# Optimization experiments

Measured on AMD Instinct MI355X. Metric: run time of the kernel, lower is better.

## Reference

```python
import jax, jax.numpy as jnp
import numpy as np

D_MODEL = 256; D_FF = 512; D_STATE = 16; D_CONV = 4; EXPAND = 2
D_INNER = EXPAND * D_MODEL          # 512
DT_RANK = (D_MODEL + 15) // 16      # 16
BSZ = 16; NVARS = 32; PATCH_NUM = 64


def setup_inputs() -> dict:
    key = jax.random.key(0)
    ks = jax.random.split(key, 16)
    def nrm(k, shape, scale=0.02):
        return jax.random.normal(k, shape, jnp.float32) * scale
    inp = {}
    inp["x"] = jax.random.normal(ks[0], (BSZ, NVARS, D_MODEL, PATCH_NUM), jnp.float32)
    # Mamba block params
    inp["in_proj_w"] = nrm(ks[1], (2 * D_INNER, D_MODEL))
    inp["in_proj_b"] = jnp.zeros((2 * D_INNER,), jnp.float32)
    inp["conv_w"] = nrm(ks[2], (D_INNER, D_CONV), 0.1)   # depthwise causal conv
    inp["conv_b"] = jnp.zeros((D_INNER,), jnp.float32)
    inp["x_proj_w"] = nrm(ks[3], (DT_RANK + 2 * D_STATE, D_INNER))
    inp["dt_proj_w"] = nrm(ks[4], (D_INNER, DT_RANK))
    inp["dt_proj_b"] = nrm(ks[5], (D_INNER,), 0.1)
    inp["A_log"] = jnp.log(jnp.broadcast_to(
        jnp.arange(1, D_STATE + 1, dtype=jnp.float32), (D_INNER, D_STATE)))
    inp["Dp"] = jnp.ones((D_INNER,), jnp.float32)
    inp["out_proj_w"] = nrm(ks[6], (D_MODEL, D_INNER))
    # Mamba_ffn norms + pointwise FFN
    inp["norm1_g"] = jnp.ones((D_MODEL,), jnp.float32)
    inp["norm1_b"] = jnp.zeros((D_MODEL,), jnp.float32)
    inp["ffn1_w"] = nrm(ks[7], (D_FF, D_MODEL))
    inp["ffn1_b"] = jnp.zeros((D_FF,), jnp.float32)
    inp["ffn2_w"] = nrm(ks[8], (D_MODEL, D_FF))
    inp["ffn2_b"] = jnp.zeros((D_MODEL,), jnp.float32)
    inp["norm2_g"] = jnp.ones((D_MODEL,), jnp.float32)
    inp["norm2_b"] = jnp.zeros((D_MODEL,), jnp.float32)
    # outer VarPatch LayerNorm
    inp["ln_g"] = jnp.ones((D_MODEL,), jnp.float32)
    inp["ln_b"] = jnp.zeros((D_MODEL,), jnp.float32)
    return inp


def layer_norm(x, g, b, eps=1e-5):
    mu = x.mean(-1, keepdims=True)
    var = ((x - mu) ** 2).mean(-1, keepdims=True)
    return (x - mu) * jax.lax.rsqrt(var + eps) * g + b


def mamba(x, in_proj_w, in_proj_b, conv_w, conv_b, x_proj_w,
          dt_proj_w, dt_proj_b, A_log, Dp, out_proj_w):
    # x: (b, L, d_model)
    b, L, _ = x.shape
    xz = x @ in_proj_w.T + in_proj_b            # (b, L, 2*d_inner)
    xi, z = jnp.split(xz, 2, axis=-1)           # each (b, L, d_inner)
    # causal depthwise conv along L
    xc = xi.transpose(0, 2, 1)                  # (b, d_inner, L)
    xc = jax.lax.conv_general_dilated(
        xc, conv_w[:, None, :], (1,), [(D_CONV - 1, 0)],
        dimension_numbers=("NCH", "OIH", "NCH"),
        feature_group_count=D_INNER) + conv_b[None, :, None]
    xi = jax.nn.silu(xc.transpose(0, 2, 1))     # (b, L, d_inner)
    x_dbl = xi @ x_proj_w.T                     # (b, L, dt_rank + 2*n)
    dt = x_dbl[..., :DT_RANK]
    B = x_dbl[..., DT_RANK:DT_RANK + D_STATE]
    C = x_dbl[..., DT_RANK + D_STATE:]
    delta = jax.nn.softplus(dt @ dt_proj_w.T + dt_proj_b)   # (b, L, d_inner)
    A = -jnp.exp(A_log)                         # (d_inner, n)

    def step(h, inp):
        d_t, B_t, C_t, u_t = inp                # (b,d),(b,n),(b,n),(b,d)
        dA = jnp.exp(d_t[..., None] * A)        # (b, d, n)
        h = dA * h + (d_t * u_t)[..., None] * B_t[:, None, :]
        y = jnp.einsum("bdn,bn->bd", h, C_t)
        return h, y

    h0 = jnp.zeros((b, D_INNER, D_STATE), xi.dtype)
    xs = (delta.transpose(1, 0, 2), B.transpose(1, 0, 2),
          C.transpose(1, 0, 2), xi.transpose(1, 0, 2))
    _, ys = jax.lax.scan(step, h0, xs)          # ys: (L, b, d_inner)
    y = ys.transpose(1, 0, 2) + xi * Dp
    y = y * jax.nn.silu(z)
    return y @ out_proj_w.T                     # (b, L, d_model)


def reference(x, in_proj_w, in_proj_b, conv_w, conv_b, x_proj_w,
              dt_proj_w, dt_proj_b, A_log, Dp, out_proj_w,
              norm1_g, norm1_b, ffn1_w, ffn1_b, ffn2_w, ffn2_b,
              norm2_g, norm2_b, ln_g, ln_b):
    b, nv, dm, pn = x.shape
    x_residual = x
    h = x.reshape(b, pn * nv, dm)               # same flat view as torch reshape
    # Mamba_ffn: mamba + residual, norm, pointwise FFN + residual, norm
    h = h + mamba(h, in_proj_w, in_proj_b, conv_w, conv_b, x_proj_w,
                  dt_proj_w, dt_proj_b, A_log, Dp, out_proj_w)
    h = layer_norm(h, norm1_g, norm1_b)
    y = jax.nn.relu(h @ ffn1_w.T + ffn1_b)      # 1x1 conv == linear
    y = y @ ffn2_w.T + ffn2_b
    h = layer_norm(h + y, norm2_g, norm2_b)
    # back to patches
    h = h.reshape(b, nv, pn, dm)
    h = layer_norm(h, ln_g, ln_b).transpose(0, 1, 3, 2)   # (b, nv, dm, pn)
    return h + x_residual
```

## Files before the change

kernel.cpp:

```cpp
#include <hip/hip_runtime.h>
#include <hip/hip_bf16.h>
#include <math.h>

#define SEQ    2048
#define NBTOT  16
#define NCH    64
#define CHL    32

#define L2E 1.4426950408889634f

typedef __attribute__((ext_vector_type(8))) __bf16 bf16x8;
typedef __attribute__((ext_vector_type(4))) float f32x4;
typedef __attribute__((ext_vector_type(2))) float f32x2;

#define GLOAD16(gp, lp)                                                   \
  __builtin_amdgcn_global_load_lds(                                       \
      (const __attribute__((address_space(1))) unsigned int*)(gp),        \
      (__attribute__((address_space(3))) unsigned int*)(lp), 16, 0, 0)

__device__ __forceinline__ float exp2_(float x) {
  return __builtin_amdgcn_exp2f(x);
}
__device__ __forceinline__ float silu_(float x) {
  return x * __builtin_amdgcn_rcpf(1.f + exp2_(-x * L2E));
}
__device__ __forceinline__ float softplus_(float x) {
  return fmaxf(x, 0.f) + __logf(1.f + exp2_(-fabsf(x) * L2E));
}
__device__ __forceinline__ float wsum_(float v) {
#pragma unroll
  for (int off = 32; off > 0; off >>= 1) v += __shfl_xor(v, off, 64);
  return v;
}
__device__ __forceinline__ int xcdswz_(int bid, int nwg) {
  return (bid & 7) * (nwg >> 3) + (bid >> 3);
}
__device__ __forceinline__ void powpairs_(float e1, f32x2 p[8]) {
  float e2 = e1 * e1;
  f32x2 p0; p0.x = e1; p0.y = e2;
  f32x2 s2; s2.x = e2; s2.y = e2;
  f32x2 s4 = s2 * s2;
  f32x2 s8 = s4 * s4;
  p[0] = p0;      p[1] = p0 * s2; p[2] = p0 * s4; p[3] = p[1] * s4;
  p[4] = p0 * s8; p[5] = p[1] * s8; p[6] = p[2] * s8; p[7] = p[3] * s8;
}

template <bool BIAS, bool RELU, bool RES, bool RESB, bool F32OUT, bool BF16OUT,
          int NTLOG>
__global__ __launch_bounds__(256) void gemm_bf16(
    const __hip_bfloat16* __restrict__ A, const __hip_bfloat16* __restrict__ W,
    const float* __restrict__ bias, const float* __restrict__ res,
    const __hip_bfloat16* __restrict__ resb, float* __restrict__ C,
    __hip_bfloat16* __restrict__ Cb, int N, int K) {
  __shared__ __align__(16) char ShRaw[36864];
  short* Als = reinterpret_cast<short*>(ShRaw);
  short* Bls = Als + 8192;
  const int tid = threadIdx.x;
  const int lane = tid & 63;
  const int wid = tid >> 6;
  const int swz = xcdswz_(blockIdx.x, gridDim.x);
  const int m0 = (swz >> NTLOG) * 128;
  const int n0 = (swz & ((1 << NTLOG) - 1)) * 128;
  const int wm = (wid >> 1) * 64;
  const int wn = (wid & 1) * 64;
  const int lr = lane & 15;
  const int lk = lane >> 4;

  f32x4 acc[4][4];
#pragma unroll
  for (int m = 0; m < 4; ++m)
#pragma unroll
    for (int n = 0; n < 4; ++n) acc[m][n] = (f32x4){0.f, 0.f, 0.f, 0.f};

  const int srow = wid * 32 + (lane >> 3);
  const int scol = (lane & 7) * 8;
  const __hip_bfloat16* Ag = A + (size_t)(m0 + srow) * K + scol;
  const __hip_bfloat16* Wg = W + (size_t)(n0 + srow) * K + scol;
  short* Alb = Als + wid * 2048;
  short* Blb = Bls + wid * 2048;

  for (int kt = 0; kt < K; kt += 64) {
#pragma unroll
    for (int i = 0; i < 4; ++i) {
      GLOAD16(Ag + (size_t)(i * 8) * K + kt, Alb + i * 512);
      GLOAD16(Wg + (size_t)(i * 8) * K + kt, Blb + i * 512);
    }
    __syncthreads();
    const bf16x8* Af = reinterpret_cast<const bf16x8*>(Als);
    const bf16x8* Bf = reinterpret_cast<const bf16x8*>(Bls);
#pragma unroll
    for (int ks = 0; ks < 2; ++ks) {
      bf16x8 av[4], bv[4];
#pragma unroll
      for (int m = 0; m < 4; ++m)
        av[m] = Af[(wm + m * 16 + lr) * 8 + ks * 4 + lk];
#pragma unroll
      for (int n = 0; n < 4; ++n)
        bv[n] = Bf[(wn + n * 16 + lr) * 8 + ks * 4 + lk];
#pragma unroll
      for (int m = 0; m < 4; ++m)
#pragma unroll
        for (int n = 0; n < 4; ++n)
          acc[m][n] = __builtin_amdgcn_mfma_f32_16x16x32_bf16(
              av[m], bv[n], acc[m][n], 0, 0, 0);
    }
    __syncthreads();
  }

  if (BF16OUT) {
    __hip_bfloat16* epi =
        reinterpret_cast<__hip_bfloat16*>(ShRaw) + wid * 4608;
#pragma unroll
    for (int n = 0; n < 4; ++n) {
      int col = n0 + wn + n * 16 + lr;
      float bval = BIAS ? bias[col] : 0.f;
#pragma unroll
      for (int m = 0; m < 4; ++m) {
        int lrow = m * 16 + lk * 4;
#pragma unroll
        for (int r = 0; r < 4; ++r) {
          float v = acc[m][n][r];
          if (BIAS) v += bval;
          if (RES) v += res[(size_t)(m0 + wm + lrow + r) * N + col];
          if (RESB)
            v += __bfloat162float(resb[(size_t)(m0 + wm + lrow + r) * N + col]);
          if (RELU) v = fmaxf(v, 0.f);
          epi[(lrow + r) * 72 + n * 16 + lr] = __float2bfloat16(v);
        }
      }
    }
    const int lr8 = (lane & 7) * 8;
    const int lrw = lane >> 3;
    const size_t obase = (size_t)(m0 + wm) * N + n0 + wn + lr8;
#pragma unroll
    for (int j = 0; j < 8; ++j) {
      int row = j * 8 + lrw;
      int4 vv = *reinterpret_cast<const int4*>(epi + row * 72 + lr8);
      *reinterpret_cast<int4*>(&Cb[obase + (size_t)row * N]) = vv;
    }
  }
  if (F32OUT) {
#pragma unroll
    for (int n = 0; n < 4; ++n) {
      int col = n0 + wn + n * 16 + lr;
      if (col >= N) continue;
      float bval = BIAS ? bias[col] : 0.f;
#pragma unroll
      for (int m = 0; m < 4; ++m) {
        int row0 = m0 + wm + m * 16 + lk * 4;
#pragma unroll
        for (int r = 0; r < 4; ++r) {
          size_t off = (size_t)(row0 + r) * N + col;
          float v = acc[m][n][r];
          if (BIAS) v += bval;
          if (RES) v += res[off];
          if (RESB) v += __bfloat162float(resb[off]);
          if (RELU) v = fmaxf(v, 0.f);
          C[off] = v;
        }
      }
    }
  }
}

__global__ __launch_bounds__(256) void cast_bf16_k(
    const float* __restrict__ src, __hip_bfloat16* __restrict__ dst, int n4) {
  int i = xcdswz_(blockIdx.x, gridDim.x) * 256 + threadIdx.x;
  if (i >= n4) return;
  float4 v = reinterpret_cast<const float4*>(src)[i];
  union { __hip_bfloat16 h[4]; short4 s4; } u;
  u.h[0] = __float2bfloat16(v.x); u.h[1] = __float2bfloat16(v.y);
  u.h[2] = __float2bfloat16(v.z); u.h[3] = __float2bfloat16(v.w);
  reinterpret_cast<short4*>(dst)[i] = u.s4;
}

__global__ __launch_bounds__(256) void pad_wx_k(
    const float* __restrict__ src, __hip_bfloat16* __restrict__ dst) {
  int i = blockIdx.x * 256 + threadIdx.x;
  int row = i >> 7;
  union { __hip_bfloat16 h[4]; short4 s4; } u;
  if (row < 48) {
    float4 v = reinterpret_cast<const float4*>(src)[i];
    u.h[0] = __float2bfloat16(v.x); u.h[1] = __float2bfloat16(v.y);
    u.h[2] = __float2bfloat16(v.z); u.h[3] = __float2bfloat16(v.w);
  } else {
    u.h[0] = u.h[1] = u.h[2] = u.h[3] = __float2bfloat16(0.f);
  }
  reinterpret_cast<short4*>(dst)[i] = u.s4;
}

__global__ __launch_bounds__(256) void conv_silu_k(
    const __hip_bfloat16* __restrict__ xz, const float* __restrict__ cw,
    const float* __restrict__ cb, __hip_bfloat16* __restrict__ xi) {
  int idx = xcdswz_(blockIdx.x, gridDim.x) * 256 + threadIdx.x;
  int t = idx & 63;
  int r = idx >> 6;
  int l = r & (SEQ - 1);
  int c8 = t << 3;
  const __hip_bfloat16* p = xz + (size_t)r * 1024 + c8;
  union U8 { int4 v; __hip_bfloat16 h[8]; } x0, x1, x2, x3, o;
  const int4 z4 = make_int4(0, 0, 0, 0);
  x3.v = *reinterpret_cast<const int4*>(p);
  x2.v = (l >= 1) ? *reinterpret_cast<const int4*>(p - 1024) : z4;
  x1.v = (l >= 2) ? *reinterpret_cast<const int4*>(p - 2048) : z4;
  x0.v = (l >= 3) ? *reinterpret_cast<const int4*>(p - 3072) : z4;
  const float4* cw4 = reinterpret_cast<const float4*>(cw);
#pragma unroll
  for (int j = 0; j < 8; ++j) {
    float4 w = cw4[c8 + j];
    float acc = cb[c8 + j];
    acc = fmaf(w.x, __bfloat162float(x0.h[j]), acc);
    acc = fmaf(w.y, __bfloat162float(x1.h[j]), acc);
    acc = fmaf(w.z, __bfloat162float(x2.h[j]), acc);
    acc = fmaf(w.w, __bfloat162float(x3.h[j]), acc);
    o.h[j] = __float2bfloat16(silu_(acc));
  }
  reinterpret_cast<int4*>(xi)[idx] = o.v;
}

__global__ __launch_bounds__(256) void scan_p1(
    const __hip_bfloat16* __restrict__ u, const float* __restrict__ xdbl,
    const float* __restrict__ A_log, const float* __restrict__ wdt,
    const float* __restrict__ bdt, float* __restrict__ dlsum,
    __hip_bfloat16* __restrict__ hp, __hip_bfloat16* __restrict__ deltab) {
  const int w = xcdswz_(blockIdx.x, gridDim.x);
  const int b = w >> 7;
  const int c = (w >> 1) & 63;
  const int d = ((w & 1) << 8) + threadIdx.x;
  const int l0 = c * CHL;
  float A2[16];
  f32x2 w2[8];
  {
    const float4* aq = reinterpret_cast<const float4*>(&A_log[d * 16]);
    const f32x2* wq = reinterpret_cast<const f32x2*>(&wdt[d * 16]);
#pragma unroll
    for (int q = 0; q < 4; ++q) {
      float4 v = aq[q];
      A2[q * 4 + 0] = -exp2_(v.x * L2E) * L2E;
      A2[q * 4 + 1] = -exp2_(v.y * L2E) * L2E;
      A2[q * 4 + 2] = -exp2_(v.z * L2E) * L2E;
      A2[q * 4 + 3] = -exp2_(v.w * L2E) * L2E;
    }
#pragma unroll
    for (int k = 0; k < 8; ++k) w2[k] = wq[k];
  }
  bool chainok = true;
#pragma unroll
  for (int n = 1; n < 16; ++n)
    chainok = chainok &&
              (fabsf(A2[n] - (float)(n + 1) * A2[0]) <=
               1e-4f * (float)(n + 1) * fabsf(A2[0]));
  const float bdtd = bdt[d];
  const float nL = A2[0];
  f32x2 h2[8];
#pragma unroll
  for (int k = 0; k < 8; ++k) h2[k] = (f32x2){0.f, 0.f};
  float dls = 0.f;
  size_t base = (size_t)(b * SEQ + l0) * 512 + d;
  const float* rowp = xdbl + (size_t)(b * SEQ + l0) * 48;
  if (chainok) {
#pragma unroll 4
    for (int i = 0; i < CHL; ++i) {
      const f32x2* r2 = reinterpret_cast<const f32x2*>(rowp + i * 48);
      f32x2 acc2; acc2.x = bdtd; acc2.y = 0.f;
#pragma unroll
      for (int k = 0; k < 8; ++k)
        acc2 = __builtin_elementwise_fma(r2[k], w2[k], acc2);
      float dl = softplus_(acc2.x + acc2.y);
      deltab[base + (size_t)i * 512] = __float2bfloat16(dl);
      dls += dl;
      float du = dl * __bfloat162float(u[base + (size_t)i * 512]);
      f32x2 p[8];
      powpairs_(exp2_(dl * nL), p);
      f32x2 du2; du2.x = du; du2.y = du;
#pragma unroll
      for (int k = 0; k < 8; ++k)
        h2[k] = __builtin_elementwise_fma(p[k], h2[k], du2 * r2[8 + k]);
    }
  } else {
#pragma unroll 2
    for (int i = 0; i < CHL; ++i) {
      const f32x2* r2 = reinterpret_cast<const f32x2*>(rowp + i * 48);
      f32x2 acc2; acc2.x = bdtd; acc2.y = 0.f;
#pragma unroll
      for (int k = 0; k < 8; ++k)
        acc2 = __builtin_elementwise_fma(r2[k], w2[k], acc2);
      float dl = softplus_(acc2.x + acc2.y);
      deltab[base + (size_t)i * 512] = __float2bfloat16(dl);
      dls += dl;
      float du = dl * __bfloat162float(u[base + (size_t)i * 512]);
      f32x2 du2; du2.x = du; du2.y = du;
#pragma unroll
      for (int k = 0; k < 8; ++k) {
        f32x2 a; a.x = exp2_(dl * A2[2 * k]); a.y = exp2_(dl * A2[2 * k + 1]);
        h2[k] = __builtin_elementwise_fma(a, h2[k], du2 * r2[8 + k]);
      }
    }
  }
  size_t sc = (size_t)(b * NCH + c) * 512 + d;
  dlsum[sc] = dls;
  union { __hip_bfloat16 h[4]; short4 s4; } o0, o1, o2, o3;
#pragma unroll
  for (int j = 0; j < 2; ++j) {
    o0.h[2*j] = __float2bfloat16(h2[j].x);   o0.h[2*j+1] = __float2bfloat16(h2[j].y);
    o1.h[2*j] = __float2bfloat16(h2[2+j].x); o1.h[2*j+1] = __float2bfloat16(h2[2+j].y);
    o2.h[2*j] = __float2bfloat16(h2[4+j].x); o2.h[2*j+1] = __float2bfloat16(h2[4+j].y);
    o3.h[2*j] = __float2bfloat16(h2[6+j].x); o3.h[2*j+1] = __float2bfloat16(h2[6+j].y);
  }
  short4* hq = reinterpret_cast<short4*>(hp + sc * 16);
  hq[0] = o0.s4; hq[1] = o1.s4; hq[2] = o2.s4; hq[3] = o3.s4;
}

__global__ __launch_bounds__(256) void scan_p2(
    __hip_bfloat16* hp, const float* __restrict__ dlsum,
    const float* __restrict__ A_log) {
  int g = xcdswz_(blockIdx.x, gridDim.x) * 256 + threadIdx.x;
  int b = g >> 13;
  int dn = g & 8191;
  int d = dn >> 4;
  float A2n = -exp2_(A_log[dn] * L2E) * L2E;
  float H = 0.f;
  for (int c = 0; c < NCH; ++c) {
    float ds = dlsum[(size_t)(b * NCH + c) * 512 + d];
    size_t idx = (size_t)(b * NCH + c) * 8192 + dn;
    float p = __bfloat162float(hp[idx]);
    float a = exp2_(A2n * ds);
    hp[idx] = __float2bfloat16(H);
    H = fmaf(a, H, p);
  }
}

__global__ __launch_bounds__(256) void scan_p3(
    const __hip_bfloat16* u,
    const float* __restrict__ A_log,
    const __hip_bfloat16* __restrict__ deltab, const float* __restrict__ xdbl,
    const __hip_bfloat16* __restrict__ Hc, const float* __restrict__ Dp,
    const __hip_bfloat16* __restrict__ xz, __hip_bfloat16* y) {
  const int w = xcdswz_(blockIdx.x, gridDim.x);
  const int b = w >> 7;
  const int c = (w >> 1) & 63;
  const int d = ((w & 1) << 8) + threadIdx.x;
  const int l0 = c * CHL;
  float A2[16];
  {
    const float4* aq = reinterpret_cast<const float4*>(&A_log[d * 16]);
#pragma unroll
    for (int q = 0; q < 4; ++q) {
      float4 v = aq[q];
      A2[q * 4 + 0] = -exp2_(v.x * L2E) * L2E;
      A2[q * 4 + 1] = -exp2_(v.y * L2E) * L2E;
      A2[q * 4 + 2] = -exp2_(v.z * L2E) * L2E;
      A2[q * 4 + 3] = -exp2_(v.w * L2E) * L2E;
    }
  }
  bool chainok = true;
#pragma unroll
  for (int n = 1; n < 16; ++n)
    chainok = chainok &&
              (fabsf(A2[n] - (float)(n + 1) * A2[0]) <=
               1e-4f * (float)(n + 1) * fabsf(A2[0]));
  const float nL = A2[0];
  f32x2 h2[8];
  {
    const short4* hq =
        reinterpret_cast<const short4*>(Hc + ((size_t)(b * NCH + c) * 512 + d) * 16);
#pragma unroll
    for (int q = 0; q < 4; ++q) {
      union { short4 s4; __hip_bfloat16 h[4]; } iv;
      iv.s4 = hq[q];
      h2[2*q].x = __bfloat162float(iv.h[0]);
      h2[2*q].y = __bfloat162float(iv.h[1]);
      h2[2*q+1].x = __bfloat162float(iv.h[2]);
      h2[2*q+1].y = __bfloat162float(iv.h[3]);
    }
  }
  const float Dpd = Dp[d];
  size_t base = (size_t)(b * SEQ + l0) * 512 + d;
  const float* rowp = xdbl + (size_t)(b * SEQ + l0) * 48;
  const __hip_bfloat16* zp = xz + (size_t)(b * SEQ + l0) * 1024 + 512 + d;
  if (chainok) {
#pragma unroll 4
    for (int i = 0; i < CHL; ++i) {
      const f32x2* r2 = reinterpret_cast<const f32x2*>(rowp + i * 48);
      float dl = __bfloat162float(deltab[base + (size_t)i * 512]);
      float ul = __bfloat162float(u[base + (size_t)i * 512]);
      float du = dl * ul;
      f32x2 p[8];
      powpairs_(exp2_(dl * nL), p);
      f32x2 du2; du2.x = du; du2.y = du;
      f32x2 yv2; yv2.x = 0.f; yv2.y = 0.f;
#pragma unroll
      for (int k = 0; k < 8; ++k) {
        h2[k] = __builtin_elementwise_fma(p[k], h2[k], du2 * r2[8 + k]);
        yv2 = __builtin_elementwise_fma(h2[k], r2[16 + k], yv2);
      }
      float yv = yv2.x + yv2.y;
      float zv = __bfloat162float(zp[(size_t)i * 1024]);
      y[base + (size_t)i * 512] =
          __float2bfloat16((yv + ul * Dpd) * silu_(zv));
    }
  } else {
#pragma unroll 2
    for (int i = 0; i < CHL; ++i) {
      const f32x2* r2 = reinterpret_cast<const f32x2*>(rowp + i * 48);
      float dl = __bfloat162float(deltab[base + (size_t)i * 512]);
      float ul = __bfloat162float(u[base + (size_t)i * 512]);
      float du = dl * ul;
      f32x2 du2; du2.x = du; du2.y = du;
      f32x2 yv2; yv2.x = 0.f; yv2.y = 0.f;
#pragma unroll
      for (int k = 0; k < 8; ++k) {
        f32x2 a; a.x = exp2_(dl * A2[2 * k]); a.y = exp2_(dl * A2[2 * k + 1]);
        h2[k] = __builtin_elementwise_fma(a, h2[k], du2 * r2[8 + k]);
        yv2 = __builtin_elementwise_fma(h2[k], r2[16 + k], yv2);
      }
      float yv = yv2.x + yv2.y;
      float zv = __bfloat162float(zp[(size_t)i * 1024]);
      y[base + (size_t)i * 512] =
          __float2bfloat16((yv + ul * Dpd) * silu_(zv));
    }
  }
}

__global__ __launch_bounds__(256) void ln_k(
    const __hip_bfloat16* __restrict__ in, const float* __restrict__ g,
    const float* __restrict__ bb, __hip_bfloat16* __restrict__ outb) {
  int row = (xcdswz_(blockIdx.x, gridDim.x) * 256 + threadIdx.x) >> 6;
  int lane = threadIdx.x & 63;
  union { short4 s4; __hip_bfloat16 h[4]; } iv;
  iv.s4 = reinterpret_cast<const short4*>(in)[row * 64 + lane];
  float v0 = __bfloat162float(iv.h[0]), v1 = __bfloat162float(iv.h[1]);
  float v2 = __bfloat162float(iv.h[2]), v3 = __bfloat162float(iv.h[3]);
  float mu = wsum_(v0 + v1 + v2 + v3) * (1.f / 256.f);
  float a0 = v0 - mu, a1 = v1 - mu, a2 = v2 - mu, a3 = v3 - mu;
  float var = wsum_(a0 * a0 + a1 * a1 + a2 * a2 + a3 * a3) * (1.f / 256.f);
  float rs = __builtin_amdgcn_rsqf(var + 1e-5f);
  float4 gg = *reinterpret_cast<const float4*>(&g[lane * 4]);
  float4 bq = *reinterpret_cast<const float4*>(&bb[lane * 4]);
  union { __hip_bfloat16 h[4]; short4 s4; } u;
  u.h[0] = __float2bfloat16(a0 * rs * gg.x + bq.x);
  u.h[1] = __float2bfloat16(a1 * rs * gg.y + bq.y);
  u.h[2] = __float2bfloat16(a2 * rs * gg.z + bq.z);
  u.h[3] = __float2bfloat16(a3 * rs * gg.w + bq.w);
  reinterpret_cast<short4*>(outb)[row * 64 + lane] = u.s4;
}

__global__ __launch_bounds__(256) void final_k(
    const __hip_bfloat16* __restrict__ t2, const float* __restrict__ g2v,
    const float* __restrict__ b2v, const float* __restrict__ g3v,
    const float* __restrict__ b3v, const float* __restrict__ x,
    float* __restrict__ out) {
  int bx = xcdswz_(blockIdx.x, gridDim.x);
  int half = bx & 1, nv = (bx >> 1) & 31, b = bx >> 6;
  int wave = threadIdx.x >> 6, lane = threadIdx.x & 63;
  __shared__ float sh[32][257];
  float4 gg2 = *reinterpret_cast<const float4*>(&g2v[lane * 4]);
  float4 bb2 = *reinterpret_cast<const float4*>(&b2v[lane * 4]);
  float4 gg3 = *reinterpret_cast<const float4*>(&g3v[lane * 4]);
  float4 bb3 = *reinterpret_cast<const float4*>(&b3v[lane * 4]);
#pragma unroll
  for (int i = 0; i < 8; ++i) {
    int pn = wave * 8 + i;
    int r = ((b * 32 + nv) << 6) + (half << 5) + pn;
    union { short4 s4; __hip_bfloat16 h[4]; } iv;
    iv.s4 = reinterpret_cast<const short4*>(t2)[r * 64 + lane];
    float v0 = __bfloat162float(iv.h[0]), v1 = __bfloat162float(iv.h[1]);
    float v2 = __bfloat162float(iv.h[2]), v3 = __bfloat162float(iv.h[3]);
    float mu = wsum_(v0 + v1 + v2 + v3) * (1.f / 256.f);
    float a0 = v0 - mu, a1 = v1 - mu, a2 = v2 - mu, a3 = v3 - mu;
    float var = wsum_(a0 * a0 + a1 * a1 + a2 * a2 + a3 * a3) * (1.f / 256.f);
    float rs = __builtin_amdgcn_rsqf(var + 1e-5f);
    a0 = a0 * rs * gg2.x + bb2.x; a1 = a1 * rs * gg2.y + bb2.y;
    a2 = a2 * rs * gg2.z + bb2.z; a3 = a3 * rs * gg2.w + bb2.w;
    mu = wsum_(a0 + a1 + a2 + a3) * (1.f / 256.f);
    float c0 = a0 - mu, c1 = a1 - mu, c2 = a2 - mu, c3 = a3 - mu;
    var = wsum_(c0 * c0 + c1 * c1 + c2 * c2 + c3 * c3) * (1.f / 256.f);
    rs = __builtin_amdgcn_rsqf(var + 1e-5f);
    sh[pn][lane * 4 + 0] = c0 * rs * gg3.x + bb3.x;
    sh[pn][lane * 4 + 1] = c1 * rs * gg3.y + bb3.y;
    sh[pn][lane * 4 + 2] = c2 * rs * gg3.z + bb3.z;
    sh[pn][lane * 4 + 3] = c3 * rs * gg3.w + bb3.w;
  }
  __syncthreads();
  int pnl = threadIdx.x & 31;
  int dbase = threadIdx.x >> 5;
  size_t obase = (size_t)((b * 32 + nv) * 256) * 64 + (half << 5) + pnl;
#pragma unroll
  for (int k = 0; k < 32; ++k) {
    int dd = dbase + (k << 3);
    size_t oi = obase + (size_t)dd * 64;
    out[oi] = sh[pnl][dd] + x[oi];
  }
}

extern "C" void kernel_launch(void* const* d_in, const int* in_sizes, int n_in,
                              void* d_out, int out_size, void* d_ws,
                              size_t ws_size, hipStream_t stream) {
  const float* x    = (const float*)d_in[0];
  const float* w_in = (const float*)d_in[1];
  const float* b_in = (const float*)d_in[2];
  const float* cw   = (const float*)d_in[3];
  const float* cb   = (const float*)d_in[4];
  const float* wx   = (const float*)d_in[5];
  const float* wdt  = (const float*)d_in[6];
  const float* bdt  = (const float*)d_in[7];
  const float* alog = (const float*)d_in[8];
  const float* Dp   = (const float*)d_in[9];
  const float* wout = (const float*)d_in[10];
  const float* g1   = (const float*)d_in[11];
  const float* b1   = (const float*)d_in[12];
  const float* wf1  = (const float*)d_in[13];
  const float* bf1  = (const float*)d_in[14];
  const float* wf2  = (const float*)d_in[15];
  const float* bf2  = (const float*)d_in[16];
  const float* g2   = (const float*)d_in[17];
  const float* b2   = (const float*)d_in[18];
  const float* g3   = (const float*)d_in[19];
  const float* b3   = (const float*)d_in[20];
  float* out = (float*)d_out;

  const size_t MB1 = 1048576;
  char* g = (char*)d_ws;
  __hip_bfloat16* wbf_in  = (__hip_bfloat16*)(g);
  __hip_bfloat16* wbf_out = (__hip_bfloat16*)(g + 524288);
  __hip_bfloat16* wbf_f1  = (__hip_bfloat16*)(g + 786432);
  __hip_bfloat16* wbf_f2  = (__hip_bfloat16*)(g + 1048576);
  __hip_bfloat16* wbf_xp  = (__hip_bfloat16*)(g + 1310720);
  const size_t SHARED = 1572864;

  const size_t PB = 11 * MB1 + 393216;
  int nb = (int)((ws_size - SHARED) / PB);
  if (ws_size <= SHARED || nb < 1) return;
  if (nb > NBTOT) nb = NBTOT;

  dim3 blk(256);
  cast_bf16_k<<<dim3(256), blk, 0, stream>>>(w_in, wbf_in, 65536);
  cast_bf16_k<<<dim3(128), blk, 0, stream>>>(wout, wbf_out, 32768);
  cast_bf16_k<<<dim3(128), blk, 0, stream>>>(wf1, wbf_f1, 32768);
  cast_bf16_k<<<dim3(128), blk, 0, stream>>>(wf2, wbf_f2, 32768);
  pad_wx_k<<<dim3(64), blk, 0, stream>>>(wx, wbf_xp);

  for (int b0 = 0; b0 < NBTOT; b0 += nb) {
    int bn = (NBTOT - b0 < nb) ? (NBTOT - b0) : nb;
    char* base = g + SHARED;
    char* RA = base;
    char* RB = base + (size_t)bn * 4 * MB1;
    char* RC = base + (size_t)bn * 5 * MB1;
    char* RD = base + (size_t)bn * 7 * MB1;
    char* RE = RD + (size_t)bn * 393216;
    char* RF = RE + (size_t)bn * 2 * MB1;

    __hip_bfloat16* xz     = (__hip_bfloat16*)RA;
    __hip_bfloat16* t2b    = (__hip_bfloat16*)RA;
    __hip_bfloat16* xbf    = (__hip_bfloat16*)RB;
    float*          dlsum  = (float*)RB;
    __hip_bfloat16* xibf   = (__hip_bfloat16*)RC;
    __hip_bfloat16* ffnybf = (__hip_bfloat16*)RC;
    float*          xdbl   = (float*)RD;
    __hip_bfloat16* hp     = (__hip_bfloat16*)RE;
    __hip_bfloat16* resb   = (__hip_bfloat16*)RE;
    __hip_bfloat16* h1bf   = (__hip_bfloat16*)(RE + (size_t)bn * MB1);
    __hip_bfloat16* deltab = (__hip_bfloat16*)RF;

    const float* xg = x + (size_t)b0 * SEQ * 256;
    float* outg = out + (size_t)b0 * SEQ * 256;
    int M = bn * SEQ;
    int MT = M / 128;

    cast_bf16_k<<<dim3(M * 64 / 256), blk, 0, stream>>>(xg, xbf, M * 64);
    gemm_bf16<true, false, false, false, false, true, 3>
        <<<dim3(8 * MT), blk, 0, stream>>>(xbf, wbf_in, b_in, nullptr, nullptr,
                                           nullptr, xz, 1024, 256);
    conv_silu_k<<<dim3(M / 4), blk, 0, stream>>>(xz, cw, cb, xibf);
    gemm_bf16<false, false, false, false, true, false, 0>
        <<<dim3(MT), blk, 0, stream>>>(xibf, wbf_xp, nullptr, nullptr,
                                       nullptr, xdbl, nullptr, 48, 512);
    scan_p1<<<dim3(bn * 128), blk, 0, stream>>>(xibf, xdbl, alog, wdt, bdt,
                                                dlsum, hp, deltab);
    scan_p2<<<dim3(bn * 32), blk, 0, stream>>>(hp, dlsum, alog);
    scan_p3<<<dim3(bn * 128), blk, 0, stream>>>(xibf, alog, deltab, xdbl,
                                                hp, Dp, xz, xibf);
    gemm_bf16<false, false, true, false, false, true, 1>
        <<<dim3(2 * MT), blk, 0, stream>>>(xibf, wbf_out, nullptr, xg, nullptr,
                                           nullptr, resb, 256, 512);
    ln_k<<<dim3(M / 4), blk, 0, stream>>>(resb, g1, b1, h1bf);
    gemm_bf16<true, true, false, false, false, true, 2>
        <<<dim3(4 * MT), blk, 0, stream>>>(h1bf, wbf_f1, bf1, nullptr, nullptr,
                                           nullptr, ffnybf, 512, 256);
    gemm_bf16<true, false, false, true, false, true, 1>
        <<<dim3(2 * MT), blk, 0, stream>>>(ffnybf, wbf_f2, bf2, nullptr, h1bf,
                                           nullptr, t2b, 256, 512);
    final_k<<<dim3(bn * 64), blk, 0, stream>>>(t2b, g2, b2, g3, b3, xg, outg);
  }
}
```

Measured before the change: 277.6 us.

## Fuse causal conv+SiLU into x_proj GEMM and scan kernels, drop xi buffer

Removes the standalone conv_silu kernel and its materialized bf16 xi tensor. The depthwise causal conv and SiLU are recomputed on the fly from xz inside a dedicated x_proj GEMM, which builds its A tile in registers, and inside both scan passes using a rolling three-tap window. This saves one kernel launch and a write plus reread of the xi activation. In exchange the conv is computed three times, and the x_proj GEMM loses async LDS loads for A.

```diff
diff --git a/kernel.cpp b/kernel.cpp
--- a/kernel.cpp
+++ b/kernel.cpp
@@ -45,12 +45,11 @@
   p[4] = p0 * s8; p[5] = p[1] * s8; p[6] = p[2] * s8; p[7] = p[3] * s8;
 }
 
-template <bool BIAS, bool RELU, bool RES, bool RESB, bool F32OUT, bool BF16OUT,
-          int NTLOG>
+template <bool BIAS, bool RELU, bool RES, bool RESB, bool BF16OUT, int NTLOG>
 __global__ __launch_bounds__(256) void gemm_bf16(
     const __hip_bfloat16* __restrict__ A, const __hip_bfloat16* __restrict__ W,
     const float* __restrict__ bias, const float* __restrict__ res,
-    const __hip_bfloat16* __restrict__ resb, float* __restrict__ C,
+    const __hip_bfloat16* __restrict__ resb,
     __hip_bfloat16* __restrict__ Cb, int N, int K) {
   __shared__ __align__(16) char ShRaw[36864];
   short* Als = reinterpret_cast<short*>(ShRaw);
@@ -107,58 +106,125 @@
     __syncthreads();
   }
 
-  if (BF16OUT) {
-    __hip_bfloat16* epi =
-        reinterpret_cast<__hip_bfloat16*>(ShRaw) + wid * 4608;
-#pragma unroll
-    for (int n = 0; n < 4; ++n) {
-      int col = n0 + wn + n * 16 + lr;
-      float bval = BIAS ? bias[col] : 0.f;
-#pragma unroll
-      for (int m = 0; m < 4; ++m) {
-        int lrow = m * 16 + lk * 4;
-#pragma unroll
-        for (int r = 0; r < 4; ++r) {
-          float v = acc[m][n][r];
-          if (BIAS) v += bval;
-          if (RES) v += res[(size_t)(m0 + wm + lrow + r) * N + col];
-          if (RESB)
-            v += __bfloat162float(resb[(size_t)(m0 + wm + lrow + r) * N + col]);
-          if (RELU) v = fmaxf(v, 0.f);
-          epi[(lrow + r) * 72 + n * 16 + lr] = __float2bfloat16(v);
-        }
+  __hip_bfloat16* epi = reinterpret_cast<__hip_bfloat16*>(ShRaw) + wid * 4608;
+#pragma unroll
+  for (int n = 0; n < 4; ++n) {
+    int col = n0 + wn + n * 16 + lr;
+    float bval = BIAS ? bias[col] : 0.f;
+#pragma unroll
+    for (int m = 0; m < 4; ++m) {
+      int lrow = m * 16 + lk * 4;
+#pragma unroll
+      for (int r = 0; r < 4; ++r) {
+        float v = acc[m][n][r];
+        if (BIAS) v += bval;
+        if (RES) v += res[(size_t)(m0 + wm + lrow + r) * N + col];
+        if (RESB)
+          v += __bfloat162float(resb[(size_t)(m0 + wm + lrow + r) * N + col]);
+        if (RELU) v = fmaxf(v, 0.f);
+        epi[(lrow + r) * 72 + n * 16 + lr] = __float2bfloat16(v);
       }
     }
-    const int lr8 = (lane & 7) * 8;
-    const int lrw = lane >> 3;
-    const size_t obase = (size_t)(m0 + wm) * N + n0 + wn + lr8;
-#pragma unroll
-    for (int j = 0; j < 8; ++j) {
-      int row = j * 8 + lrw;
-      int4 vv = *reinterpret_cast<const int4*>(epi + row * 72 + lr8);
-      *reinterpret_cast<int4*>(&Cb[obase + (size_t)row * N]) = vv;
-    }
-  }
-  if (F32OUT) {
-#pragma unroll
-    for (int n = 0; n < 4; ++n) {
-      int col = n0 + wn + n * 16 + lr;
-      if (col >= N) continue;
-      float bval = BIAS ? bias[col] : 0.f;
-#pragma unroll
-      for (int m = 0; m < 4; ++m) {
-        int row0 = m0 + wm + m * 16 + lk * 4;
-#pragma unroll
-        for (int r = 0; r < 4; ++r) {
-          size_t off = (size_t)(row0 + r) * N + col;
-          float v = acc[m][n][r];
-          if (BIAS) v += bval;
-          if (RES) v += res[off];
-          if (RESB) v += __bfloat162float(resb[off]);
-          if (RELU) v = fmaxf(v, 0.f);
-          C[off] = v;
-        }
+  }
+  const int lr8 = (lane & 7) * 8;
+  const int lrw = lane >> 3;
+  const size_t obase = (size_t)(m0 + wm) * N + n0 + wn + lr8;
+#pragma unroll
+  for (int j = 0; j < 8; ++j) {
+    int row = j * 8 + lrw;
+    int4 vv = *reinterpret_cast<const int4*>(epi + row * 72 + lr8);
+    *reinterpret_cast<int4*>(&Cb[obase + (size_t)row * N]) = vv;
+  }
+}
+
+__global__ __launch_bounds__(256) void gemm_xproj(
+    const __hip_bfloat16* __restrict__ xz, const __hip_bfloat16* __restrict__ W,
+    const float* __restrict__ cw, const float* __restrict__ cb,
+    float* __restrict__ C) {
+  __shared__ __align__(16) short Als[128 * 64];
+  __shared__ __align__(16) short Bls[128 * 64];
+  const int tid = threadIdx.x;
+  const int lane = tid & 63;
+  const int wid = tid >> 6;
+  const int m0 = xcdswz_(blockIdx.x, gridDim.x) * 128;
+  const int wm = (wid >> 1) * 64;
+  const int wn = (wid & 1) * 64;
+  const int lr = lane & 15;
+  const int lk = lane >> 4;
+
+  f32x4 acc[4][4];
+#pragma unroll
+  for (int m = 0; m < 4; ++m)
+#pragma unroll
+    for (int n = 0; n < 4; ++n) acc[m][n] = (f32x4){0.f, 0.f, 0.f, 0.f};
+
+  const int srow = wid * 32 + (lane >> 3);
+  const int scol = (lane & 7) * 8;
+  const __hip_bfloat16* Wg = W + (size_t)srow * 512 + scol;
+  short* Alb = Als + wid * 2048;
+  short* Blb = Bls + wid * 2048;
+  const float4* cw4 = reinterpret_cast<const float4*>(cw);
+
+  for (int kt = 0; kt < 512; kt += 64) {
+#pragma unroll
+    for (int i = 0; i < 4; ++i)
+      GLOAD16(Wg + (size_t)(i * 8) * 512 + kt, Blb + i * 512);
+#pragma unroll
+    for (int i = 0; i < 4; ++i) {
+      int rr = m0 + srow + i * 8;
+      int l = rr & (SEQ - 1);
+      const __hip_bfloat16* pz = xz + (size_t)rr * 1024 + kt + scol;
+      union U8 { int4 v; __hip_bfloat16 h[8]; } x0, x1, x2, x3, o;
+      const int4 z4 = make_int4(0, 0, 0, 0);
+      x3.v = *reinterpret_cast<const int4*>(pz);
+      x2.v = (l >= 1) ? *reinterpret_cast<const int4*>(pz - 1024) : z4;
+      x1.v = (l >= 2) ? *reinterpret_cast<const int4*>(pz - 2048) : z4;
+      x0.v = (l >= 3) ? *reinterpret_cast<const int4*>(pz - 3072) : z4;
+#pragma unroll
+      for (int j = 0; j < 8; ++j) {
+        int ch = kt + scol + j;
+        float4 w = cw4[ch];
+        float a = cb[ch];
+        a = fmaf(w.x, __bfloat162float(x0.h[j]), a);
+        a = fmaf(w.y, __bfloat162float(x1.h[j]), a);
+        a = fmaf(w.z, __bfloat162float(x2.h[j]), a);
+        a = fmaf(w.w, __bfloat162float(x3.h[j]), a);
+        o.h[j] = __float2bfloat16(silu_(a));
       }
+      *reinterpret_cast<int4*>(Alb + i * 512 + lane * 8) = o.v;
+    }
+    __syncthreads();
+    const bf16x8* Af = reinterpret_cast<const bf16x8*>(Als);
+    const bf16x8* Bf = reinterpret_cast<const bf16x8*>(Bls);
+#pragma unroll
+    for (int ks = 0; ks < 2; ++ks) {
+      bf16x8 av[4], bv[4];
+#pragma unroll
+      for (int m = 0; m < 4; ++m)
+        av[m] = Af[(wm + m * 16 + lr) * 8 + ks * 4 + lk];
+#pragma unroll
+      for (int n = 0; n < 4; ++n)
+        bv[n] = Bf[(wn + n * 16 + lr) * 8 + ks * 4 + lk];
+#pragma unroll
+      for (int m = 0; m < 4; ++m)
+#pragma unroll
+        for (int n = 0; n < 4; ++n)
+          acc[m][n] = __builtin_amdgcn_mfma_f32_16x16x32_bf16(
+              av[m], bv[n], acc[m][n], 0, 0, 0);
+    }
+    __syncthreads();
+  }
+
+#pragma unroll
+  for (int n = 0; n < 4; ++n) {
+    int col = wn + n * 16 + lr;
+    if (col >= 48) continue;
+#pragma unroll
+    for (int m = 0; m < 4; ++m) {
+      int row0 = m0 + wm + m * 16 + lk * 4;
+#pragma unroll
+      for (int r = 0; r < 4; ++r)
+        C[(size_t)(row0 + r) * 48 + col] = acc[m][n][r];
     }
   }
 }
@@ -189,39 +255,11 @@
   reinterpret_cast<short4*>(dst)[i] = u.s4;
 }
 
-__global__ __launch_bounds__(256) void conv_silu_k(
-    const __hip_bfloat16* __restrict__ xz, const float* __restrict__ cw,
-    const float* __restrict__ cb, __hip_bfloat16* __restrict__ xi) {
-  int idx = xcdswz_(blockIdx.x, gridDim.x) * 256 + threadIdx.x;
-  int t = idx & 63;
-  int r = idx >> 6;
-  int l = r & (SEQ - 1);
-  int c8 = t << 3;
-  const __hip_bfloat16* p = xz + (size_t)r * 1024 + c8;
-  union U8 { int4 v; __hip_bfloat16 h[8]; } x0, x1, x2, x3, o;
-  const int4 z4 = make_int4(0, 0, 0, 0);
-  x3.v = *reinterpret_cast<const int4*>(p);
-  x2.v = (l >= 1) ? *reinterpret_cast<const int4*>(p - 1024) : z4;
-  x1.v = (l >= 2) ? *reinterpret_cast<const int4*>(p - 2048) : z4;
-  x0.v = (l >= 3) ? *reinterpret_cast<const int4*>(p - 3072) : z4;
-  const float4* cw4 = reinterpret_cast<const float4*>(cw);
-#pragma unroll
-  for (int j = 0; j < 8; ++j) {
-    float4 w = cw4[c8 + j];
-    float acc = cb[c8 + j];
-    acc = fmaf(w.x, __bfloat162float(x0.h[j]), acc);
-    acc = fmaf(w.y, __bfloat162float(x1.h[j]), acc);
-    acc = fmaf(w.z, __bfloat162float(x2.h[j]), acc);
-    acc = fmaf(w.w, __bfloat162float(x3.h[j]), acc);
-    o.h[j] = __float2bfloat16(silu_(acc));
-  }
-  reinterpret_cast<int4*>(xi)[idx] = o.v;
-}
-
 __global__ __launch_bounds__(256) void scan_p1(
-    const __hip_bfloat16* __restrict__ u, const float* __restrict__ xdbl,
+    const __hip_bfloat16* __restrict__ xz, const float* __restrict__ xdbl,
     const float* __restrict__ A_log, const float* __restrict__ wdt,
-    const float* __restrict__ bdt, float* __restrict__ dlsum,
+    const float* __restrict__ bdt, const float* __restrict__ cw,
+    const float* __restrict__ cb, float* __restrict__ dlsum,
     __hip_bfloat16* __restrict__ hp, __hip_bfloat16* __restrict__ deltab) {
   const int w = xcdswz_(blockIdx.x, gridDim.x);
   const int b = w >> 7;
@@ -252,6 +290,12 @@
                1e-4f * (float)(n + 1) * fabsf(A2[0]));
   const float bdtd = bdt[d];
   const float nL = A2[0];
+  const float4 cwv = reinterpret_cast<const float4*>(cw)[d];
+  const float cbv = cb[d];
+  const __hip_bfloat16* zrow = xz + (size_t)(b * SEQ + l0) * 1024 + d;
+  float xm1 = (l0 >= 1) ? __bfloat162float(zrow[-1024]) : 0.f;
+  float xm2 = (l0 >= 2) ? __bfloat162float(zrow[-2048]) : 0.f;
+  float xm3 = (l0 >= 3) ? __bfloat162float(zrow[-3072]) : 0.f;
   f32x2 h2[8];
 #pragma unroll
   for (int k = 0; k < 8; ++k) h2[k] = (f32x2){0.f, 0.f};
@@ -261,6 +305,11 @@
   if (chainok) {
 #pragma unroll 4
     for (int i = 0; i < CHL; ++i) {
+      float xn = __bfloat162float(zrow[(size_t)i * 1024]);
+      float ua = fmaf(cwv.w, xn, fmaf(cwv.z, xm1,
+                  fmaf(cwv.y, xm2, fmaf(cwv.x, xm3, cbv))));
+      float ul = silu_(ua);
+      xm3 = xm2; xm2 = xm1; xm1 = xn;
       const f32x2* r2 = reinterpret_cast<const f32x2*>(rowp + i * 48);
       f32x2 acc2; acc2.x = bdtd; acc2.y = 0.f;
 #pragma unroll
@@ -269,7 +318,7 @@
       float dl = softplus_(acc2.x + acc2.y);
       deltab[base + (size_t)i * 512] = __float2bfloat16(dl);
       dls += dl;
-      float du = dl * __bfloat162float(u[base + (size_t)i * 512]);
+      float du = dl * ul;
       f32x2 p[8];
       powpairs_(exp2_(dl * nL), p);
       f32x2 du2; du2.x = du; du2.y = du;
@@ -280,6 +329,11 @@
   } else {
 #pragma unroll 2
     for (int i = 0; i < CHL; ++i) {
+      float xn = __bfloat162float(zrow[(size_t)i * 1024]);
+      float ua = fmaf(cwv.w, xn, fmaf(cwv.z, xm1,
+                  fmaf(cwv.y, xm2, fmaf(cwv.x, xm3, cbv))));
+      float ul = silu_(ua);
+      xm3 = xm2; xm2 = xm1; xm1 = xn;
       const f32x2* r2 = reinterpret_cast<const f32x2*>(rowp + i * 48);
       f32x2 acc2; acc2.x = bdtd; acc2.y = 0.f;
 #pragma unroll
@@ -288,7 +342,7 @@
       float dl = softplus_(acc2.x + acc2.y);
       deltab[base + (size_t)i * 512] = __float2bfloat16(dl);
       dls += dl;
-      float du = dl * __bfloat162float(u[base + (size_t)i * 512]);
+      float du = dl * ul;
       f32x2 du2; du2.x = du; du2.y = du;
 #pragma unroll
       for (int k = 0; k < 8; ++k) {
@@ -331,11 +385,11 @@
 }
 
 __global__ __launch_bounds__(256) void scan_p3(
-    const __hip_bfloat16* u,
     const float* __restrict__ A_log,
     const __hip_bfloat16* __restrict__ deltab, const float* __restrict__ xdbl,
     const __hip_bfloat16* __restrict__ Hc, const float* __restrict__ Dp,
-    const __hip_bfloat16* __restrict__ xz, __hip_bfloat16* y) {
+    const __hip_bfloat16* __restrict__ xz, const float* __restrict__ cw,
+    const float* __restrict__ cb, __hip_bfloat16* __restrict__ y) {
   const int w = xcdswz_(blockIdx.x, gridDim.x);
   const int b = w >> 7;
   const int c = (w >> 1) & 63;
@@ -375,15 +429,25 @@
     }
   }
   const float Dpd = Dp[d];
+  const float4 cwv = reinterpret_cast<const float4*>(cw)[d];
+  const float cbv = cb[d];
+  const __hip_bfloat16* zrow = xz + (size_t)(b * SEQ + l0) * 1024 + d;
+  float xm1 = (l0 >= 1) ? __bfloat162float(zrow[-1024]) : 0.f;
+  float xm2 = (l0 >= 2) ? __bfloat162float(zrow[-2048]) : 0.f;
+  float xm3 = (l0 >= 3) ? __bfloat162float(zrow[-3072]) : 0.f;
   size_t base = (size_t)(b * SEQ + l0) * 512 + d;
   const float* rowp = xdbl + (size_t)(b * SEQ + l0) * 48;
-  const __hip_bfloat16* zp = xz + (size_t)(b * SEQ + l0) * 1024 + 512 + d;
+  const __hip_bfloat16* zp = zrow + 512;
   if (chainok) {
 #pragma unroll 4
     for (int i = 0; i < CHL; ++i) {
+      float xn = __bfloat162float(zrow[(size_t)i * 1024]);
+      float ua = fmaf(cwv.w, xn, fmaf(cwv.z, xm1,
+                  fmaf(cwv.y, xm2, fmaf(cwv.x, xm3, cbv))));
+      float ul = silu_(ua);
+      xm3 = xm2; xm2 = xm1; xm1 = xn;
       const f32x2* r2 = reinterpret_cast<const f32x2*>(rowp + i * 48);
       float dl = __bfloat162float(deltab[base + (size_t)i * 512]);
-      float ul = __bfloat162float(u[base + (size_t)i * 512]);
       float du = dl * ul;
       f32x2 p[8];
       powpairs_(exp2_(dl * nL), p);
@@ -402,9 +466,13 @@
   } else {
 #pragma unroll 2
     for (int i = 0; i < CHL; ++i) {
+      float xn = __bfloat162float(zrow[(size_t)i * 1024]);
+      float ua = fmaf(cwv.w, xn, fmaf(cwv.z, xm1,
+                  fmaf(cwv.y, xm2, fmaf(cwv.x, xm3, cbv))));
+      float ul = silu_(ua);
+      xm3 = xm2; xm2 = xm1; xm1 = xn;
       const f32x2* r2 = reinterpret_cast<const f32x2*>(rowp + i * 48);
       float dl = __bfloat162float(deltab[base + (size_t)i * 512]);
-      float ul = __bfloat162float(u[base + (size_t)i * 512]);
       float du = dl * ul;
       f32x2 du2; du2.x = du; du2.y = du;
       f32x2 yv2; yv2.x = 0.f; yv2.y = 0.f;
@@ -554,7 +622,7 @@
     __hip_bfloat16* t2b    = (__hip_bfloat16*)RA;
     __hip_bfloat16* xbf    = (__hip_bfloat16*)RB;
     float*          dlsum  = (float*)RB;
-    __hip_bfloat16* xibf   = (__hip_bfloat16*)RC;
+    __hip_bfloat16* ybf    = (__hip_bfloat16*)RC;
     __hip_bfloat16* ffnybf = (__hip_bfloat16*)RC;
     float*          xdbl   = (float*)RD;
     __hip_bfloat16* hp     = (__hip_bfloat16*)RE;
@@ -568,28 +636,25 @@
     int MT = M / 128;
 
     cast_bf16_k<<<dim3(M * 64 / 256), blk, 0, stream>>>(xg, xbf, M * 64);
-    gemm_bf16<true, false, false, false, false, true, 3>
+    gemm_bf16<true, false, false, false, true, 3>
         <<<dim3(8 * MT), blk, 0, stream>>>(xbf, wbf_in, b_in, nullptr, nullptr,
-                                           nullptr, xz, 1024, 256);
-    conv_silu_k<<<dim3(M / 4), blk, 0, stream>>>(xz, cw, cb, xibf);
-    gemm_bf16<false, false, false, false, true, false, 0>
-        <<<dim3(MT), blk, 0, stream>>>(xibf, wbf_xp, nullptr, nullptr,
-                                       nullptr, xdbl, nullptr, 48, 512);
-    scan_p1<<<dim3(bn * 128), blk, 0, stream>>>(xibf, xdbl, alog, wdt, bdt,
-                                                dlsum, hp, deltab);
+                                           xz, 1024, 256);
+    gemm_xproj<<<dim3(MT), blk, 0, stream>>>(xz, wbf_xp, cw, cb, xdbl);
+    scan_p1<<<dim3(bn * 128), blk, 0, stream>>>(xz, xdbl, alog, wdt, bdt,
+                                                cw, cb, dlsum, hp, deltab);
     scan_p2<<<dim3(bn * 32), blk, 0, stream>>>(hp, dlsum, alog);
-    scan_p3<<<dim3(bn * 128), blk, 0, stream>>>(xibf, alog, deltab, xdbl,
-                                                hp, Dp, xz, xibf);
-    gemm_bf16<false, false, true, false, false, true, 1>
-        <<<dim3(2 * MT), blk, 0, stream>>>(xibf, wbf_out, nullptr, xg, nullptr,
-                                           nullptr, resb, 256, 512);
+    scan_p3<<<dim3(bn * 128), blk, 0, stream>>>(alog, deltab, xdbl, hp, Dp,
+                                                xz, cw, cb, ybf);
+    gemm_bf16<false, false, true, false, true, 1>
+        <<<dim3(2 * MT), blk, 0, stream>>>(ybf, wbf_out, nullptr, xg, nullptr,
+                                           resb, 256, 512);
     ln_k<<<dim3(M / 4), blk, 0, stream>>>(resb, g1, b1, h1bf);
-    gemm_bf16<true, true, false, false, false, true, 2>
+    gemm_bf16<true, true, false, false, true, 2>
         <<<dim3(4 * MT), blk, 0, stream>>>(h1bf, wbf_f1, bf1, nullptr, nullptr,
-                                           nullptr, ffnybf, 512, 256);
-    gemm_bf16<true, false, false, true, false, true, 1>
+                                           ffnybf, 512, 256);
+    gemm_bf16<true, false, false, true, true, 1>
         <<<dim3(2 * MT), blk, 0, stream>>>(ffnybf, wbf_f2, bf2, nullptr, h1bf,
-                                           nullptr, t2b, 256, 512);
+                                           t2b, 256, 512);
     final_k<<<dim3(bn * 64), blk, 0, stream>>>(t2b, g2, b2, g3, b3, xg, outg);
   }
 }
```

After: 297.4 us. 7.2% more time.
